# Kernel tuning notes

Measured on AMD Instinct MI355X. Metric: run time of the kernel, lower is better.

## Reference

```python
import jax, jax.numpy as jnp
import numpy as np
from jax import lax

B, S, L, H, D_IN, W = 128, 64, 137, 128, 64, 256  # batch, segments, logsig_dim, hidden, input_dim, vf_width


def setup_inputs() -> dict:
    key = jax.random.key(0)
    ks = jax.random.split(key, 12)
    rn = lambda k, s, sc: jax.random.normal(k, s, dtype=jnp.float32) * sc
    return {
        "times": jnp.arange(S + 1, dtype=jnp.float32),
        "logsig": rn(ks[0], (B, S, L), 0.1),
        "initial": rn(ks[1], (B, D_IN), 1.0),
        "in_w": rn(ks[2], (D_IN, H), 0.12),
        "in_b": rn(ks[3], (H,), 0.05),
        "h1_w": rn(ks[4], (H, W), 0.09),
        "h1_b": rn(ks[5], (W,), 0.05),
        "h2_w": rn(ks[6], (W, W), 0.06),
        "h2_b": rn(ks[7], (W,), 0.05),
        "vo_w": rn(ks[8], (W, W), 0.06),
        "vo_b": rn(ks[9], (W,), 0.05),
        "ml_w": rn(ks[10], (W, H * (L - 1)), 0.02),
        "ml_b": rn(ks[11], (H * (L - 1),), 0.01),
    }


def reference(times, logsig, initial, in_w, in_b, h1_w, h1_b, h2_w, h2_b, vo_w, vo_b, ml_w, ml_b):
    intervals = times                 # [S+1]; forward requires times == registered intervals
    coeffs = logsig[:, :, 1:]         # [B, S, L-1] (first logsig channel dropped)
    h0 = initial @ in_w + in_b        # [B, H]

    def func(t, y):
        # searchsorted + clamp, exactly as in the torch module
        idx = jnp.clip(jnp.searchsorted(intervals, t, side='left'), 1, S)
        dt = intervals[idx] - intervals[idx - 1]
        coeff = jnp.take(coeffs, idx - 1, axis=1)        # [B, L-1]
        h = jax.nn.relu(y @ h1_w + h1_b)                 # vf MLP (vf_depth-1 = 2 hidden layers)
        h = jax.nn.relu(h @ h2_w + h2_b)
        h = jnp.tanh(h @ vo_w + vo_b)                    # final tanh activation
        vf = (h @ ml_w + ml_b).reshape(B, H, L - 1)      # [B, H, L-1]
        return jnp.einsum('bhd,bd->bh', vf, coeff) / dt  # [B, H]

    def step(y, n):
        # one fixed-size Heun (RK2) step from intervals[n] to intervals[n+1]
        t0, t1 = intervals[n], intervals[n + 1]
        dt = t1 - t0
        k1 = func(t0, y)
        k2 = func(t1, y + dt * k1)
        y1 = y + 0.5 * dt * (k1 + k2)
        return y1, y1

    _, ys = lax.scan(step, h0, jnp.arange(S))            # ys: [S, B, H]
    features = jnp.concatenate([h0[:, None, :], jnp.swapaxes(ys, 0, 1)], axis=1)  # [B, S+1, H]
    return features, features[:, -1]
```

## Files before the change

### kernel.cpp

```cpp
#include <hip/hip_runtime.h>
#include <hip/hip_bf16.h>


#define BB 128
#define SS 64
#define LL 137
#define HH 128
#define DIN 64
#define WW 256
#define DD 136
#define KP 160
#define NC 32768
#define OUT2_OFF ((size_t)BB*(SS+1)*HH)

typedef __hip_bfloat16 bf16;
typedef __attribute__((ext_vector_type(8))) short short8;
typedef __attribute__((ext_vector_type(4))) float f32x4;
typedef _Float16 h2t __attribute__((ext_vector_type(2)));

__device__ __forceinline__ bf16 f2bf(float x){ return __float2bfloat16(x); }

__device__ __forceinline__ float fdot2u(unsigned w, unsigned y, float acc){
#if __has_builtin(__builtin_amdgcn_fdot2)
  return __builtin_amdgcn_fdot2(__builtin_bit_cast(h2t, w),
                                __builtin_bit_cast(h2t, y), acc, false);
#else
  h2t a = __builtin_bit_cast(h2t, w), b2 = __builtin_bit_cast(h2t, y);
  return acc + (float)a[0]*(float)b2[0] + (float)a[1]*(float)b2[1];
#endif
}
__device__ __forceinline__ float dot8(uint4 w, uint4 y, float acc){
  acc = fdot2u(w.x, y.x, acc);
  acc = fdot2u(w.y, y.y, acc);
  acc = fdot2u(w.z, y.z, acc);
  acc = fdot2u(w.w, y.w, acc);
  return acc;
}

__device__ __forceinline__ float fast_tanh(float x){
  float e = __expf(2.f*x);
#if __has_builtin(__builtin_amdgcn_rcpf)
  float r = __builtin_amdgcn_rcpf(e + 1.f);
#else
  float r = 1.f/(e + 1.f);
#endif
  return 1.f - 2.f*r;
}

__global__ void prep_coeff(const float* __restrict__ logsig, bf16* __restrict__ cA){
  int m = blockIdx.x;
  int d = threadIdx.x;
  int a = m >> 7, b = m & 127;
  float v = 0.0f;
  if (d < DD) v = logsig[(size_t)(b*SS + a)*LL + 1 + d];
  cA[(size_t)m*KP + d] = f2bf(v);
}

__global__ void prep_btt(const float* __restrict__ mlw, bf16* __restrict__ btt){
  int c = blockIdx.x;
  int d = threadIdx.x;
  int w = ((c >> 10) << 3) | (c & 7);
  int h = (c >> 3) & 127;
  float v = 0.0f;
  if (d < DD) v = mlw[(size_t)w*(HH*DD) + h*DD + d];
  btt[(size_t)c*KP + d] = f2bf(v);
}

__global__ void prep_packw(const float* __restrict__ src, uint4* __restrict__ dst){
  int c = blockIdx.x, j = threadIdx.x;
  union { _Float16 h[8]; uint4 v; } u;
  #pragma unroll
  for (int r = 0; r < 8; ++r) u.h[r] = (_Float16)src[(size_t)(c*8+r)*WW + j];
  dst[c*WW + j] = u.v;
}

__global__ void abias_kernel(const float* __restrict__ mlb, const float* __restrict__ logsig,
                             float* __restrict__ Abias){
  int a = blockIdx.x, b = blockIdx.y;
  int h = threadIdx.x;
  __shared__ float cf[DD];
  for (int d = h; d < DD; d += HH) cf[d] = logsig[(size_t)(b*SS + a)*LL + 1 + d];
  __syncthreads();
  float acc = 0.f;
  const float* mb = mlb + (size_t)h*DD;
  #pragma unroll 8
  for (int d = 0; d < DD; ++d) acc += cf[d] * mb[d];
  Abias[((size_t)a*BB + b)*HH + h] = acc;
}

#define AST 40
__global__ __launch_bounds__(512) void agemm_kernel(const bf16* __restrict__ cA,
                                                    const bf16* __restrict__ btt,
                                                    _Float16* __restrict__ As, int mAbs0){
  __shared__ __align__(16) short sm[32768];
  int mt = blockIdx.x, nt = blockIdx.y;
  int t = threadIdx.x, lane = t & 63, wid = t >> 6;
  int mBlockAbs = mAbs0 + mt*128;
  int c0 = nt*256;
  int mW = (wid & 1)*64, cW = (wid >> 1)*64;
  const int mr = lane & 15, q = lane >> 4;
  const int srow = t >> 2, sseg = t & 3;

  {
    uint4 va  = *(const uint4*)(cA  + (size_t)(mBlockAbs + srow)*KP + sseg*8);
    uint4 vb0 = *(const uint4*)(btt + (size_t)(c0 + srow)*KP + sseg*8);
    uint4 vb1 = *(const uint4*)(btt + (size_t)(c0 + 128 + srow)*KP + sseg*8);
    *(uint4*)&sm[0     + srow*AST + sseg*8] = va;
    *(uint4*)&sm[10240 + srow*AST + sseg*8] = vb0;
    *(uint4*)&sm[10240 + (128 + srow)*AST + sseg*8] = vb1;
  }
  __syncthreads();

  f32x4 acc[4][4];
  #pragma unroll
  for (int i = 0; i < 4; ++i)
    #pragma unroll
    for (int j = 0; j < 4; ++j)
      acc[i][j] = (f32x4){0.f,0.f,0.f,0.f};

  #pragma unroll
  for (int kk = 0; kk < 5; ++kk){
    const int cur = kk & 1;
    const int aBase = cur ? 5120 : 0;
    const int bBase = cur ? 20480 : 10240;
    uint4 va, vb0, vb1;
    if (kk < 4){
      int d0 = (kk+1)*32;
      va  = *(const uint4*)(cA  + (size_t)(mBlockAbs + srow)*KP + d0 + sseg*8);
      vb0 = *(const uint4*)(btt + (size_t)(c0 + srow)*KP + d0 + sseg*8);
      vb1 = *(const uint4*)(btt + (size_t)(c0 + 128 + srow)*KP + d0 + sseg*8);
    }
    short8 af[4], bfr[4];
    #pragma unroll
    for (int mi = 0; mi < 4; ++mi)
      af[mi]  = *(const short8*)&sm[aBase + (mW + mi*16 + mr)*AST + q*8];
    #pragma unroll
    for (int ci = 0; ci < 4; ++ci)
      bfr[ci] = *(const short8*)&sm[bBase + (cW + ci*16 + mr)*AST + q*8];
    #pragma unroll
    for (int mi = 0; mi < 4; ++mi)
      #pragma unroll
      for (int ci = 0; ci < 4; ++ci)
        acc[mi][ci] = __builtin_amdgcn_mfma_f32_16x16x32_bf16(af[mi], bfr[ci], acc[mi][ci], 0, 0, 0);
    if (kk < 4){
      const int aN = cur ? 0 : 5120;
      const int bN = cur ? 10240 : 20480;
      *(uint4*)&sm[aN + srow*AST + sseg*8] = va;
      *(uint4*)&sm[bN + srow*AST + sseg*8] = vb0;
      *(uint4*)&sm[bN + (128 + srow)*AST + sseg*8] = vb1;
    }
    __syncthreads();
  }

  #pragma unroll
  for (int mi = 0; mi < 4; ++mi)
    #pragma unroll
    for (int ci = 0; ci < 4; ++ci){
      int col = cW + ci*16 + mr;
      #pragma unroll
      for (int r = 0; r < 4; ++r){
        int row = mW + mi*16 + q*4 + r;
        int cs = col ^ (((row >> 2) & 3) << 3);
        _Float16 hv = (_Float16)acc[mi][ci][r];
        sm[row*256 + cs] = *(short*)&hv;
      }
    }
  __syncthreads();
  int mLocBlock = mt*128;
  #pragma unroll
  for (int rep = 0; rep < 8; ++rep){
    int idx = t + rep*512;
    int row = idx >> 5, seg = idx & 31;
    int cs = (seg*8) ^ (((row >> 2) & 3) << 3);
    uint4 v = *(const uint4*)&sm[row*256 + cs];
    *(uint4*)(As + (size_t)(mLocBlock + row)*NC + c0 + seg*8) = v;
  }
}

__device__ __forceinline__ float nrde_func(
    int b, int wave, int lane,
    const uint4* __restrict__ wp1, const uint4* __restrict__ wp2,
    const uint4* vo_sm,
    const _Float16* yh, _Float16* h1h, _Float16* h2h, _Float16* h3h,
    const float* bs1, const float* bs2, const float* bsv,
    const _Float16* __restrict__ As, const float* __restrict__ Abias,
    int aLoc, int aAbs, float inv_dtf)
{
  const int j  = (wave << 4) | (lane & 15);
  const int q  = lane >> 4;
  const int h  = (wave << 3) | (lane & 7);
  const int q8 = lane >> 3;

  uint4 w1r[4], w2r[8], ar[4];
  {
    const uint4* wp = wp1 + (q << 2)*WW + j;
    #pragma unroll
    for (int cc = 0; cc < 4; ++cc) w1r[cc] = wp[cc*WW];
  }
  {
    const uint4* wp = wp2 + (q << 3)*WW + j;
    #pragma unroll
    for (int cc = 0; cc < 8; ++cc) w2r[cc] = wp[cc*WW];
  }
  {
    const uint4* Ap = (const uint4*)(As + ((size_t)aLoc*BB + b)*NC);
    #pragma unroll
    for (int cc = 0; cc < 4; ++cc) ar[cc] = Ap[((q8 << 2) + cc)*HH + h];
  }
  float ab = Abias[((size_t)aAbs*BB + b)*HH + h];

  {
    const uint4* yp = (const uint4*)yh + (q << 2);
    float a0 = 0.f, a1 = 0.f;
    a0 = dot8(w1r[0], yp[0], a0); a1 = dot8(w1r[1], yp[1], a1);
    a0 = dot8(w1r[2], yp[2], a0); a1 = dot8(w1r[3], yp[3], a1);
    float acc = a0 + a1;
    acc += __shfl_xor(acc, 16);
    acc += __shfl_xor(acc, 32);
    if (q == 0){ float v = bs1[j] + acc; h1h[j] = (_Float16)(v > 0.f ? v : 0.f); }
  }
  __syncthreads();
  {
    const uint4* hp = (const uint4*)h1h + (q << 3);
    float a0 = 0.f, a1 = 0.f;
    #pragma unroll
    for (int cc = 0; cc < 8; cc += 2){
      a0 = dot8(w2r[cc],   hp[cc],   a0);
      a1 = dot8(w2r[cc+1], hp[cc+1], a1);
    }
    float acc = a0 + a1;
    acc += __shfl_xor(acc, 16);
    acc += __shfl_xor(acc, 32);
    if (q == 0){ float v = bs2[j] + acc; h2h[j] = (_Float16)(v > 0.f ? v : 0.f); }
  }
  __syncthreads();
  {
    const uint4* wp = vo_sm + (q << 3)*WW + j;
    const uint4* hp = (const uint4*)h2h + (q << 3);
    float a0 = 0.f, a1 = 0.f;
    #pragma unroll
    for (int cc = 0; cc < 8; cc += 2){
      a0 = dot8(wp[cc*WW],     hp[cc],   a0);
      a1 = dot8(wp[(cc+1)*WW], hp[cc+1], a1);
    }
    float acc = a0 + a1;
    acc += __shfl_xor(acc, 16);
    acc += __shfl_xor(acc, 32);
    if (q == 0) h3h[j] = (_Float16)fast_tanh(bsv[j] + acc);
  }
  __syncthreads();
  {
    const uint4* hp = (const uint4*)h3h + (q8 << 2);
    float a0 = 0.f, a1 = 0.f;
    a0 = dot8(ar[0], hp[0], a0); a1 = dot8(ar[1], hp[1], a1);
    a0 = dot8(ar[2], hp[2], a0); a1 = dot8(ar[3], hp[3], a1);
    float acc = a0 + a1;
    acc += __shfl_xor(acc, 8);
    acc += __shfl_xor(acc, 16);
    acc += __shfl_xor(acc, 32);
    return (acc + ab) * inv_dtf;
  }
}

__global__ __launch_bounds__(1024) void scan_kernel(
    const float* __restrict__ times, const float* __restrict__ initial,
    const float* __restrict__ in_w, const float* __restrict__ in_b,
    const float* __restrict__ h1_b, const float* __restrict__ h2_b,
    const float* __restrict__ vo_b,
    const uint4* __restrict__ wp1, const uint4* __restrict__ wp2,
    const uint4* __restrict__ wpv,
    const _Float16* __restrict__ As, const float* __restrict__ Abias,
    float* __restrict__ y_state, float* __restrict__ out,
    int s0, int s1, int aBase)
{
  __shared__ __align__(16) uint4 vo_sm[32*WW];
  __shared__ __align__(16) _Float16 yh[HH];
  __shared__ __align__(16) _Float16 h1h[WW];
  __shared__ __align__(16) _Float16 h2h[WW];
  __shared__ __align__(16) _Float16 h3h[WW];
  __shared__ float yv[HH];
  __shared__ float bs1[WW], bs2[WW], bsv[WW];

  const int b = blockIdx.x, t = threadIdx.x;
  const int wave = t >> 6, lane = t & 63;
  const int h = (wave << 3) | (lane & 7);
  const bool tail = (lane >> 3) == 0;

  for (int i = t; i < 32*WW; i += 1024) vo_sm[i] = wpv[i];
  if (t < WW){ bs1[t] = h1_b[t]; bs2[t] = h2_b[t]; bsv[t] = vo_b[t]; }

  if (s0 == 0){
    if (t < HH){
      float acc = in_b[t];
      for (int i = 0; i < DIN; ++i)
        acc += initial[b*DIN + i] * in_w[(size_t)i*HH + t];
      yv[t] = acc; yh[t] = (_Float16)acc;
      out[(size_t)b*(SS+1)*HH + t] = acc;
    }
  } else if (t < HH){
    float v = y_state[b*HH + t];
    yv[t] = v; yh[t] = (_Float16)v;
  }
  __syncthreads();

  for (int n = s0; n < s1; ++n){
    float t0v = times[n], t1v = times[n+1];
    float dt = t1v - t0v;
    int idx1 = (n >= 1) ? n : 1;
    float dtf1 = times[idx1] - times[idx1-1];
    int a1 = (n >= 1) ? (n-1) : 0;
    float k1 = nrde_func(b, wave, lane, wp1, wp2, vo_sm, yh, h1h, h2h, h3h,
                         bs1, bs2, bsv, As, Abias, a1 - aBase, a1, 1.f/dtf1);
    if (tail) yh[h] = (_Float16)(yv[h] + dt*k1);
    __syncthreads();
    float k2 = nrde_func(b, wave, lane, wp1, wp2, vo_sm, yh, h1h, h2h, h3h,
                         bs1, bs2, bsv, As, Abias, n - aBase, n, 1.f/dt);
    if (tail){
      float ynew = yv[h] + 0.5f*dt*(k1 + k2);
      yv[h] = ynew; yh[h] = (_Float16)ynew;
      out[((size_t)b*(SS+1) + (n+1))*HH + h] = ynew;
    }
    __syncthreads();
  }

  if (tail){
    y_state[b*HH + h] = yv[h];
    if (s1 == SS) out[OUT2_OFF + (size_t)b*HH + h] = yv[h];
  }
}

extern "C" void kernel_launch(void* const* d_in, const int* in_sizes, int n_in,
                              void* d_out, int out_size, void* d_ws, size_t ws_size,
                              hipStream_t stream)
{
  (void)in_sizes; (void)n_in; (void)out_size;
  const float* times   = (const float*)d_in[0];
  const float* logsig  = (const float*)d_in[1];
  const float* initial = (const float*)d_in[2];
  const float* in_w    = (const float*)d_in[3];
  const float* in_b    = (const float*)d_in[4];
  const float* h1_w    = (const float*)d_in[5];
  const float* h1_b    = (const float*)d_in[6];
  const float* h2_w    = (const float*)d_in[7];
  const float* h2_b    = (const float*)d_in[8];
  const float* vo_w    = (const float*)d_in[9];
  const float* vo_b    = (const float*)d_in[10];
  const float* ml_w    = (const float*)d_in[11];
  const float* ml_b    = (const float*)d_in[12];
  float* out = (float*)d_out;

  char* ws = (char*)d_ws;
  size_t off = 0;
  bf16* cA      = (bf16*)(ws + off); off += (size_t)8192*KP*2;
  bf16* btt     = (bf16*)(ws + off); off += (size_t)NC*KP*2;
  float* Abias  = (float*)(ws + off); off += (size_t)SS*BB*HH*4;
  float* y_state= (float*)(ws + off); off += (size_t)BB*HH*4;
  uint4* wp1    = (uint4*)(ws + off); off += (size_t)16*WW*16;
  uint4* wp2    = (uint4*)(ws + off); off += (size_t)32*WW*16;
  uint4* wpv    = (uint4*)(ws + off); off += (size_t)32*WW*16;
  _Float16* As  = (_Float16*)(ws + off);
  size_t perA = (size_t)BB*HH*WW*2;
  size_t avail = (ws_size > off) ? (ws_size - off) : 0;
  int C = (int)(avail / perA);
  if (C > SS) C = SS;
  if (C < 2) return;

  prep_coeff<<<8192, 160, 0, stream>>>(logsig, cA);
  prep_btt<<<NC, 160, 0, stream>>>(ml_w, btt);
  abias_kernel<<<dim3(SS, BB), HH, 0, stream>>>(ml_b, logsig, Abias);
  prep_packw<<<16, WW, 0, stream>>>(h1_w, wp1);
  prep_packw<<<32, WW, 0, stream>>>(h2_w, wp2);
  prep_packw<<<32, WW, 0, stream>>>(vo_w, wpv);

  int s = 0, aB = 0;
  while (s < SS){
    int cc = SS - aB; if (cc > C) cc = C;
    agemm_kernel<<<dim3(cc, 128), 512, 0, stream>>>(cA, btt, As, aB*BB);
    int sEnd = aB + cc; if (sEnd > SS) sEnd = SS;
    scan_kernel<<<BB, 1024, 0, stream>>>(times, initial, in_w, in_b,
        h1_b, h2_b, vo_b, wp1, wp2, wpv, As, Abias, y_state, out, s, sEnd, aB);
    s = sEnd;
    aB = sEnd - 1;
  }
}
```

Measured before the change: 724.5 us.

## Reorder GEMM operands k-major, load whole K into LDS, hoist scan weights

The coefficient and ml_w operand buffers are now stored k-chunk-major so each 16-byte chunk of 128 rows is contiguous. The A-GEMM loads the full K=160 slab into 80KB of LDS at once, dropping the per-k double-buffering and its barriers. The output tile shrinks from 256 to 128 columns, giving twice as many blocks. Separately, the scan kernel loads its per-thread h1/h2 weight fragments into registers once, instead of reloading them from global memory on every function evaluation. The larger LDS footprint may lower occupancy, and the hoisted weights raise register pressure.

```diff
diff --git a/kernel.cpp b/kernel.cpp
--- a/kernel.cpp
+++ b/kernel.cpp
@@ -53,7 +53,8 @@
   int a = m >> 7, b = m & 127;
   float v = 0.0f;
   if (d < DD) v = logsig[(size_t)(b*SS + a)*LL + 1 + d];
-  cA[(size_t)m*KP + d] = f2bf(v);
+  int kk = d >> 5, q = (d >> 3) & 3, jj = d & 7;
+  cA[(((size_t)(kk*4 + q))*8192 + m)*8 + jj] = f2bf(v);
 }
 
 __global__ void prep_btt(const float* __restrict__ mlw, bf16* __restrict__ btt){
@@ -63,7 +64,8 @@
   int h = (c >> 3) & 127;
   float v = 0.0f;
   if (d < DD) v = mlw[(size_t)w*(HH*DD) + h*DD + d];
-  btt[(size_t)c*KP + d] = f2bf(v);
+  int kk = d >> 5, q = (d >> 3) & 3, jj = d & 7;
+  btt[(((size_t)(kk*4 + q))*NC + c)*8 + jj] = f2bf(v);
 }
 
 __global__ void prep_packw(const float* __restrict__ src, uint4* __restrict__ dst){
@@ -88,98 +90,87 @@
   Abias[((size_t)a*BB + b)*HH + h] = acc;
 }
 
-#define AST 40
 __global__ __launch_bounds__(512) void agemm_kernel(const bf16* __restrict__ cA,
                                                     const bf16* __restrict__ btt,
                                                     _Float16* __restrict__ As, int mAbs0){
-  __shared__ __align__(16) short sm[32768];
+  __shared__ __align__(16) char smb[81920];
+  short* sm = (short*)smb;
   int mt = blockIdx.x, nt = blockIdx.y;
   int t = threadIdx.x, lane = t & 63, wid = t >> 6;
   int mBlockAbs = mAbs0 + mt*128;
-  int c0 = nt*256;
-  int mW = (wid & 1)*64, cW = (wid >> 1)*64;
-  const int mr = lane & 15, q = lane >> 4;
-  const int srow = t >> 2, sseg = t & 3;
-
-  {
-    uint4 va  = *(const uint4*)(cA  + (size_t)(mBlockAbs + srow)*KP + sseg*8);
-    uint4 vb0 = *(const uint4*)(btt + (size_t)(c0 + srow)*KP + sseg*8);
-    uint4 vb1 = *(const uint4*)(btt + (size_t)(c0 + 128 + srow)*KP + sseg*8);
-    *(uint4*)&sm[0     + srow*AST + sseg*8] = va;
-    *(uint4*)&sm[10240 + srow*AST + sseg*8] = vb0;
-    *(uint4*)&sm[10240 + (128 + srow)*AST + sseg*8] = vb1;
-  }
-  __syncthreads();
-
-  f32x4 acc[4][4];
-  #pragma unroll
-  for (int i = 0; i < 4; ++i)
+  int c0 = nt*128;
+  int mW = (wid & 3)*32, cW = (wid >> 2)*64;
+  const uint4* aK = (const uint4*)cA;
+  const uint4* bK = (const uint4*)btt;
+
+  uint4 va[5], vb[5];
+  #pragma unroll
+  for (int r = 0; r < 5; ++r){
+    int lin = t + r*512;
+    int kq = lin >> 7;
+    int row = lin & 127;
+    va[r] = aK[(size_t)kq*8192 + mBlockAbs + row];
+    vb[r] = bK[(size_t)kq*NC + c0 + row];
+  }
+  #pragma unroll
+  for (int r = 0; r < 5; ++r){
+    int lin = t + r*512;
+    *(uint4*)(smb + lin*16) = va[r];
+    *(uint4*)(smb + 40960 + lin*16) = vb[r];
+  }
+  __syncthreads();
+
+  f32x4 acc[2][4];
+  #pragma unroll
+  for (int i = 0; i < 2; ++i)
     #pragma unroll
     for (int j = 0; j < 4; ++j)
       acc[i][j] = (f32x4){0.f,0.f,0.f,0.f};
 
+  const int mr = lane & 15, q = lane >> 4;
   #pragma unroll
   for (int kk = 0; kk < 5; ++kk){
-    const int cur = kk & 1;
-    const int aBase = cur ? 5120 : 0;
-    const int bBase = cur ? 20480 : 10240;
-    uint4 va, vb0, vb1;
-    if (kk < 4){
-      int d0 = (kk+1)*32;
-      va  = *(const uint4*)(cA  + (size_t)(mBlockAbs + srow)*KP + d0 + sseg*8);
-      vb0 = *(const uint4*)(btt + (size_t)(c0 + srow)*KP + d0 + sseg*8);
-      vb1 = *(const uint4*)(btt + (size_t)(c0 + 128 + srow)*KP + d0 + sseg*8);
-    }
-    short8 af[4], bfr[4];
-    #pragma unroll
-    for (int mi = 0; mi < 4; ++mi)
-      af[mi]  = *(const short8*)&sm[aBase + (mW + mi*16 + mr)*AST + q*8];
+    short8 af[2], bfr[4];
+    #pragma unroll
+    for (int mi = 0; mi < 2; ++mi)
+      af[mi]  = *(const short8*)(smb + ((size_t)((kk*4+q)*128) + mW + mi*16 + mr)*16);
     #pragma unroll
     for (int ci = 0; ci < 4; ++ci)
-      bfr[ci] = *(const short8*)&sm[bBase + (cW + ci*16 + mr)*AST + q*8];
-    #pragma unroll
-    for (int mi = 0; mi < 4; ++mi)
+      bfr[ci] = *(const short8*)(smb + 40960 + ((size_t)((kk*4+q)*128) + cW + ci*16 + mr)*16);
+    #pragma unroll
+    for (int mi = 0; mi < 2; ++mi)
       #pragma unroll
       for (int ci = 0; ci < 4; ++ci)
         acc[mi][ci] = __builtin_amdgcn_mfma_f32_16x16x32_bf16(af[mi], bfr[ci], acc[mi][ci], 0, 0, 0);
-    if (kk < 4){
-      const int aN = cur ? 0 : 5120;
-      const int bN = cur ? 10240 : 20480;
-      *(uint4*)&sm[aN + srow*AST + sseg*8] = va;
-      *(uint4*)&sm[bN + srow*AST + sseg*8] = vb0;
-      *(uint4*)&sm[bN + (128 + srow)*AST + sseg*8] = vb1;
-    }
-    __syncthreads();
-  }
-
-  #pragma unroll
-  for (int mi = 0; mi < 4; ++mi)
+  }
+  __syncthreads();
+
+  #pragma unroll
+  for (int mi = 0; mi < 2; ++mi)
     #pragma unroll
     for (int ci = 0; ci < 4; ++ci){
       int col = cW + ci*16 + mr;
       #pragma unroll
       for (int r = 0; r < 4; ++r){
         int row = mW + mi*16 + q*4 + r;
-        int cs = col ^ (((row >> 2) & 3) << 3);
         _Float16 hv = (_Float16)acc[mi][ci][r];
-        sm[row*256 + cs] = *(short*)&hv;
+        sm[row*136 + col] = *(short*)&hv;
       }
     }
   __syncthreads();
   int mLocBlock = mt*128;
   #pragma unroll
-  for (int rep = 0; rep < 8; ++rep){
+  for (int rep = 0; rep < 4; ++rep){
     int idx = t + rep*512;
-    int row = idx >> 5, seg = idx & 31;
-    int cs = (seg*8) ^ (((row >> 2) & 3) << 3);
-    uint4 v = *(const uint4*)&sm[row*256 + cs];
+    int row = idx >> 4, seg = idx & 15;
+    uint4 v = *(const uint4*)&sm[row*136 + seg*8];
     *(uint4*)(As + (size_t)(mLocBlock + row)*NC + c0 + seg*8) = v;
   }
 }
 
 __device__ __forceinline__ float nrde_func(
     int b, int wave, int lane,
-    const uint4* __restrict__ wp1, const uint4* __restrict__ wp2,
+    const uint4 (&w1r)[4], const uint4 (&w2r)[8],
     const uint4* vo_sm,
     const _Float16* yh, _Float16* h1h, _Float16* h2h, _Float16* h3h,
     const float* bs1, const float* bs2, const float* bsv,
@@ -191,17 +182,7 @@
   const int h  = (wave << 3) | (lane & 7);
   const int q8 = lane >> 3;
 
-  uint4 w1r[4], w2r[8], ar[4];
-  {
-    const uint4* wp = wp1 + (q << 2)*WW + j;
-    #pragma unroll
-    for (int cc = 0; cc < 4; ++cc) w1r[cc] = wp[cc*WW];
-  }
-  {
-    const uint4* wp = wp2 + (q << 3)*WW + j;
-    #pragma unroll
-    for (int cc = 0; cc < 8; ++cc) w2r[cc] = wp[cc*WW];
-  }
+  uint4 ar[4];
   {
     const uint4* Ap = (const uint4*)(As + ((size_t)aLoc*BB + b)*NC);
     #pragma unroll
@@ -285,9 +266,23 @@
   const int wave = t >> 6, lane = t & 63;
   const int h = (wave << 3) | (lane & 7);
   const bool tail = (lane >> 3) == 0;
+  const int j = (wave << 4) | (lane & 15);
+  const int q = lane >> 4;
 
   for (int i = t; i < 32*WW; i += 1024) vo_sm[i] = wpv[i];
   if (t < WW){ bs1[t] = h1_b[t]; bs2[t] = h2_b[t]; bsv[t] = vo_b[t]; }
+
+  uint4 w1r[4], w2r[8];
+  {
+    const uint4* wp = wp1 + (q << 2)*WW + j;
+    #pragma unroll
+    for (int cc = 0; cc < 4; ++cc) w1r[cc] = wp[cc*WW];
+  }
+  {
+    const uint4* wp = wp2 + (q << 3)*WW + j;
+    #pragma unroll
+    for (int cc = 0; cc < 8; ++cc) w2r[cc] = wp[cc*WW];
+  }
 
   if (s0 == 0){
     if (t < HH){
@@ -309,11 +304,11 @@
     int idx1 = (n >= 1) ? n : 1;
     float dtf1 = times[idx1] - times[idx1-1];
     int a1 = (n >= 1) ? (n-1) : 0;
-    float k1 = nrde_func(b, wave, lane, wp1, wp2, vo_sm, yh, h1h, h2h, h3h,
+    float k1 = nrde_func(b, wave, lane, w1r, w2r, vo_sm, yh, h1h, h2h, h3h,
                          bs1, bs2, bsv, As, Abias, a1 - aBase, a1, 1.f/dtf1);
     if (tail) yh[h] = (_Float16)(yv[h] + dt*k1);
     __syncthreads();
-    float k2 = nrde_func(b, wave, lane, wp1, wp2, vo_sm, yh, h1h, h2h, h3h,
+    float k2 = nrde_func(b, wave, lane, w1r, w2r, vo_sm, yh, h1h, h2h, h3h,
                          bs1, bs2, bsv, As, Abias, n - aBase, n, 1.f/dt);
     if (tail){
       float ynew = yv[h] + 0.5f*dt*(k1 + k2);
@@ -375,7 +370,7 @@
   int s = 0, aB = 0;
   while (s < SS){
     int cc = SS - aB; if (cc > C) cc = C;
-    agemm_kernel<<<dim3(cc, 128), 512, 0, stream>>>(cA, btt, As, aB*BB);
+    agemm_kernel<<<dim3(cc, 256), 512, 0, stream>>>(cA, btt, As, aB*BB);
     int sEnd = aB + cc; if (sEnd > SS) sEnd = SS;
     scan_kernel<<<BB, 1024, 0, stream>>>(times, initial, in_w, in_b,
         h1_b, h2_b, vo_b, wp1, wp2, wpv, As, Abias, y_state, out, s, sEnd, aB);
```

After: 641.9 us. 1.13x faster.
